# Kernel tuning notes

Measured on AMD Instinct MI355X. Metric: run time of the kernel, lower is better.

## Reference

```python
import jax, jax.numpy as jnp
import numpy as np

DIM = 1024
EXPAND = 2
HEAD_DIM = 64
D_STATE = 128
N_GROUPS = 1
D_CONV = 4
D_INNER = DIM * EXPAND            # 2048
N_HEADS = D_INNER // HEAD_DIM     # 32
CONV_DIM = D_INNER + 2 * N_GROUPS * D_STATE  # 2304
D_IN_PROJ = 2 * D_INNER + 2 * N_GROUPS * D_STATE + N_HEADS  # 4384
SEQLEN = 4096
LN_EPS = 1e-5


def setup_inputs() -> dict:
    key = jax.random.key(0)
    ks = jax.random.split(key, 6)
    x = jax.random.normal(ks[0], (SEQLEN, DIM), dtype=jnp.float32)
    W_in = jax.random.normal(ks[1], (D_IN_PROJ, DIM), dtype=jnp.float32) * 0.02
    conv_w = jax.random.normal(ks[2], (CONV_DIM, 1, D_CONV), dtype=jnp.float32) * 0.2
    conv_b = jax.random.normal(ks[3], (CONV_DIM,), dtype=jnp.float32) * 0.02
    # dt_bias init per module: dt ~ exp(U*(log(dt_max)-log(dt_min))+log(dt_min)); inv-softplus
    u = jax.random.uniform(ks[4], (N_HEADS,))
    dt = jnp.exp(u * (np.log(0.1) - np.log(0.001)) + np.log(0.001))
    dt = jnp.clip(dt, 1e-4)
    dt_bias = dt + jnp.log(-jnp.expm1(-dt))
    A_log = jnp.log(jax.random.uniform(ks[5], (N_HEADS,), minval=1.0, maxval=16.0))
    D = jnp.ones((N_HEADS,), dtype=jnp.float32)
    ln_w = jnp.ones((D_INNER,), dtype=jnp.float32)
    ln_b = jnp.zeros((D_INNER,), dtype=jnp.float32)
    W_out = jax.random.normal(jax.random.fold_in(key, 7), (DIM, D_INNER), dtype=jnp.float32) * 0.02
    return {"x": x, "W_in": W_in, "conv_w": conv_w, "conv_b": conv_b,
            "dt_bias": dt_bias, "A_log": A_log, "D": D,
            "ln_w": ln_w, "ln_b": ln_b, "W_out": W_out}


def _forward(x, W_in, conv_w, conv_b, dt_bias, A_log, D, ln_w, ln_b, W_out):
    L = x.shape[0]
    dtype = x.dtype
    A = -jnp.exp(A_log.astype(jnp.float32))  # (h,)
    zxbcdt = x @ W_in.T                       # (L, d_in_proj)
    z = zxbcdt[:, :D_INNER]                   # (L, d_inner)
    xbc = zxbcdt[:, D_INNER:D_INNER + CONV_DIM]
    dt = zxbcdt[:, -N_HEADS:]
    dt = jax.nn.softplus(dt.astype(jnp.float32) + dt_bias.astype(jnp.float32))  # (L, h)
    # depthwise 1D conv, SAME padding (module uses padding='SAME', then slices to L)
    xbc_c = jax.lax.conv_general_dilated(
        xbc.T[None],                          # (1, conv_dim, L)
        conv_w,                               # (conv_dim, 1, k)
        window_strides=(1,), padding='SAME',
        dimension_numbers=('NCH', 'OIH', 'NCH'),
        feature_group_count=CONV_DIM,
    )[0].T + conv_b                           # (L, conv_dim)
    xbc_s = jax.nn.silu(xbc_c)
    x_in = xbc_s[:, :D_INNER].reshape(L, N_HEADS, HEAD_DIM)      # (L, h, p)
    B = xbc_s[:, D_INNER:D_INNER + N_GROUPS * D_STATE]          # (L, n) with g=1
    C = xbc_s[:, D_INNER + N_GROUPS * D_STATE:]                 # (L, n)
    # non-causal linear attention (VSSD): y = C (B^T (x * dt * A)) + x * D
    dA = dt.astype(dtype) * A.astype(dtype)                     # (L, h)
    Vs = x_in * dA[..., None]                                   # (L, h, p)
    KV = jnp.einsum('ln,lhp->hnp', B, Vs)                       # (h, n, p)
    y = jnp.einsum('ln,hnp->lhp', C, KV) + x_in * D[None, :, None]
    y = y.reshape(L, D_INNER)
    # per-token LayerNorm, then multiplicative SiLU(z) gate
    mu = jnp.mean(y, axis=-1, keepdims=True)
    var = jnp.var(y, axis=-1, keepdims=True)
    yn = (y - mu) * jax.lax.rsqrt(var + LN_EPS) * ln_w + ln_b
    y = yn * jax.nn.silu(z)
    return y @ W_out.T                                          # (L, dim)


def reference(x, W_in, conv_w, conv_b, dt_bias, A_log, D, ln_w, ln_b, W_out):
    return _forward(x, W_in, conv_w, conv_b, dt_bias, A_log, D, ln_w, ln_b, W_out)
```

## Files before the change

### kernel.cpp

```cpp
#include <hip/hip_runtime.h>
#include <math.h>

#define SEQLEN    4096
#define DIM_IN    1024
#define D_INNER   2048
#define N_HEADS   32
#define D_STATE   128
#define CONV_DIM  2304
#define D_IN_PROJ 4384
#define PROJ_LD   4480
#define LN_EPS    1e-5f
#define KV_SPLIT  16

typedef __attribute__((ext_vector_type(8))) short bf16x8;
typedef __attribute__((ext_vector_type(4))) float f32x4;
typedef __attribute__((ext_vector_type(8))) short short8;

__device__ __forceinline__ ushort f2bf(float f) {
    union { float f; unsigned u; } v; v.f = f;
    unsigned u = v.u + 0x7FFFu + ((v.u >> 16) & 1u);
    return (ushort)(u >> 16);
}
__device__ __forceinline__ float bf2f(ushort h) {
    union { unsigned u; float f; } v; v.u = ((unsigned)h) << 16;
    return v.f;
}

__device__ __forceinline__ void gload16(const void* g, void* l) {
    __builtin_amdgcn_global_load_lds(
        (const __attribute__((address_space(1))) void*)g,
        (__attribute__((address_space(3))) void*)l, 16, 0, 0);
}

__global__ __launch_bounds__(256)
void cvt_bf16(const float* __restrict__ in, ushort* __restrict__ out, int n8) {
    int i = blockIdx.x * 256 + threadIdx.x;
    if (i >= n8) return;
    float4 v0 = reinterpret_cast<const float4*>(in)[i * 2];
    float4 v1 = reinterpret_cast<const float4*>(in)[i * 2 + 1];
    short8 r;
    r[0] = f2bf(v0.x); r[1] = f2bf(v0.y); r[2] = f2bf(v0.z); r[3] = f2bf(v0.w);
    r[4] = f2bf(v1.x); r[5] = f2bf(v1.y); r[6] = f2bf(v1.z); r[7] = f2bf(v1.w);
    *reinterpret_cast<short8*>(&out[i * 8]) = r;
}

__global__ __launch_bounds__(256)
void cvt_win(const float* __restrict__ in, ushort* __restrict__ out) {
    int i = blockIdx.x * 256 + threadIdx.x;
    const int n8 = PROJ_LD * DIM_IN / 8;
    if (i >= n8) return;
    int row = (i * 8) >> 10;
    short8 r;
    if (row < D_IN_PROJ) {
        float4 v0 = reinterpret_cast<const float4*>(in)[i * 2];
        float4 v1 = reinterpret_cast<const float4*>(in)[i * 2 + 1];
        r[0] = f2bf(v0.x); r[1] = f2bf(v0.y); r[2] = f2bf(v0.z); r[3] = f2bf(v0.w);
        r[4] = f2bf(v1.x); r[5] = f2bf(v1.y); r[6] = f2bf(v1.z); r[7] = f2bf(v1.w);
    } else {
        r = (short8){0,0,0,0,0,0,0,0};
    }
    *reinterpret_cast<short8*>(&out[i * 8]) = r;
}

template<int BN, int NT, int OUTBF>
__global__ __launch_bounds__(256)
void gemm_bf16_pipe(const ushort* __restrict__ A, int lda,
                    const ushort* __restrict__ B, int ldb,
                    void* __restrict__ Cout, int ldc) {
    constexpr int NI  = BN / 32;
    __shared__ ushort As[3][128 * 32];
    __shared__ ushort Bs[3][BN * 32];

    const int nwg = gridDim.x;
    const int wg  = blockIdx.x;
    const int swz = (wg & 7) * (nwg >> 3) + (wg >> 3);
    const int m0 = (swz & 31) * 128;
    const int n0 = (swz >> 5) * BN;

    const int tid  = threadIdx.x;
    const int wave = tid >> 6;
    const int lane = tid & 63;
    const int wm = (wave & 1) * 64;
    const int wn = (wave >> 1) * (BN / 2);
    const int r16 = lane & 15;
    const int kg  = lane >> 4;
    const int pkg = kg ^ ((r16 >> 1) & 3);

    f32x4 acc[4][NI];
    #pragma unroll
    for (int i = 0; i < 4; ++i)
        #pragma unroll
        for (int j = 0; j < NI; ++j) acc[i][j] = (f32x4){0.f, 0.f, 0.f, 0.f};

    const int srow = lane >> 2;
    const int scol = ((lane & 3) ^ ((lane >> 3) & 3)) * 8;
    const int ca0 = wave * 2, ca1 = wave * 2 + 1;
    const ushort* gA0 = A + (size_t)(m0 + ca0 * 16 + srow) * lda + scol;
    const ushort* gA1 = A + (size_t)(m0 + ca1 * 16 + srow) * lda + scol;
    const ushort* gB0;
    const ushort* gB1 = nullptr;
    int cb0, cb1 = 0;
    if constexpr (BN == 128) {
        cb0 = wave * 2; cb1 = wave * 2 + 1;
        gB0 = B + (size_t)(n0 + cb0 * 16 + srow) * ldb + scol;
        gB1 = B + (size_t)(n0 + cb1 * 16 + srow) * ldb + scol;
    } else {
        cb0 = wave;
        gB0 = B + (size_t)(n0 + cb0 * 16 + srow) * ldb + scol;
    }

#define STAGE_STEP(T, BUF)                                          \
    {                                                               \
        const int _k = (T) * 32;                                    \
        gload16(gA0 + _k, &As[BUF][ca0 * 512]);                     \
        gload16(gA1 + _k, &As[BUF][ca1 * 512]);                     \
        gload16(gB0 + _k, &Bs[BUF][cb0 * 512]);                     \
        if constexpr (BN == 128) gload16(gB1 + _k, &Bs[BUF][cb1 * 512]); \
    }

    STAGE_STEP(0, 0)
    STAGE_STEP(1, 1)

    int rb = 0;
    for (int t = 0; t < NT; ++t) {
        __builtin_amdgcn_sched_barrier(0);
        if (t + 1 < NT) {
            if constexpr (BN == 128) asm volatile("s_waitcnt vmcnt(4)" ::: "memory");
            else                     asm volatile("s_waitcnt vmcnt(3)" ::: "memory");
        } else {
            asm volatile("s_waitcnt vmcnt(0)" ::: "memory");
        }
        __builtin_amdgcn_s_barrier();
        __builtin_amdgcn_sched_barrier(0);

        if (t + 2 < NT) {
            int sb = rb + 2; if (sb >= 3) sb -= 3;
            STAGE_STEP(t + 2, sb)
        }

        const ushort* ab = &As[rb][0];
        const ushort* bb = &Bs[rb][0];
        bf16x8 a[4], b[NI];
        #pragma unroll
        for (int mi = 0; mi < 4; ++mi)
            a[mi] = *reinterpret_cast<const bf16x8*>(&ab[(wm + mi * 16 + r16) * 32 + pkg * 8]);
        #pragma unroll
        for (int ni = 0; ni < NI; ++ni)
            b[ni] = *reinterpret_cast<const bf16x8*>(&bb[(wn + ni * 16 + r16) * 32 + pkg * 8]);

        __builtin_amdgcn_s_setprio(1);
        #pragma unroll
        for (int mi = 0; mi < 4; ++mi)
            #pragma unroll
            for (int ni = 0; ni < NI; ++ni)
                acc[mi][ni] = __builtin_amdgcn_mfma_f32_16x16x32_bf16(a[mi], b[ni], acc[mi][ni], 0, 0, 0);
        __builtin_amdgcn_s_setprio(0);

        rb = (rb == 2) ? 0 : rb + 1;
    }
#undef STAGE_STEP

    if constexpr (OUTBF) {
        ushort* EP = &As[0][0];
        ushort* outp = (ushort*)Cout;
        __syncthreads();
        #pragma unroll
        for (int half = 0; half < 2; ++half) {
            if ((wave & 1) == half) {
                #pragma unroll
                for (int mi = 0; mi < 4; ++mi)
                    #pragma unroll
                    for (int ni = 0; ni < NI; ++ni)
                        #pragma unroll
                        for (int r = 0; r < 4; ++r)
                            EP[(mi * 16 + kg * 4 + r) * BN + wn + ni * 16 + r16] =
                                f2bf(acc[mi][ni][r]);
            }
            __syncthreads();
            #pragma unroll
            for (int i = 0; i < BN / 32; ++i) {
                int idx = tid + 256 * i;
                int row = idx / (BN / 8);
                int cb  = idx % (BN / 8);
                bf16x8 v = *reinterpret_cast<const bf16x8*>(&EP[row * BN + cb * 8]);
                *reinterpret_cast<bf16x8*>(
                    &outp[(size_t)(m0 + half * 64 + row) * ldc + n0 + cb * 8]) = v;
            }
            __syncthreads();
        }
    } else {
        float* outp = (float*)Cout;
        #pragma unroll
        for (int mi = 0; mi < 4; ++mi)
            #pragma unroll
            for (int ni = 0; ni < NI; ++ni)
                #pragma unroll
                for (int r = 0; r < 4; ++r) {
                    int row = m0 + wm + mi * 16 + kg * 4 + r;
                    int col = n0 + wn + ni * 16 + r16;
                    outp[(size_t)row * ldc + col] = acc[mi][ni][r];
                }
    }
}

__global__ __launch_bounds__(256)
void conv_silu_kernel(const ushort* __restrict__ zxb,
                      const float* __restrict__ conv_w,
                      const float* __restrict__ conv_b,
                      const float* __restrict__ dt_bias,
                      const float* __restrict__ A_log,
                      ushort* __restrict__ xbcs,
                      float* __restrict__ dA) {
    const int l = blockIdx.x;
    const ushort* base = zxb + (size_t)l * PROJ_LD + D_INNER;
    for (int c = threadIdx.x; c < CONV_DIM; c += 256) {
        float w0 = conv_w[c * 4 + 0], w1 = conv_w[c * 4 + 1];
        float w2 = conv_w[c * 4 + 2], w3 = conv_w[c * 4 + 3];
        float acc = conv_b[c];
        if (l >= 1)          acc += w0 * bf2f(base[c - PROJ_LD]);
        acc += w1 * bf2f(base[c]);
        if (l + 1 < SEQLEN)  acc += w2 * bf2f(base[c + PROJ_LD]);
        if (l + 2 < SEQLEN)  acc += w3 * bf2f(base[c + 2 * PROJ_LD]);
        float s = acc / (1.0f + expf(-acc));
        xbcs[(size_t)l * CONV_DIM + c] = f2bf(s);
    }
    if (threadIdx.x < N_HEADS) {
        int h = threadIdx.x;
        float v = bf2f(zxb[(size_t)l * PROJ_LD + (D_IN_PROJ - N_HEADS) + h]) + dt_bias[h];
        float sp = (v > 20.0f) ? v : log1pf(expf(v));
        dA[l * N_HEADS + h] = sp * (-expf(A_log[h]));
    }
}

__global__ __launch_bounds__(256)
void kv_kernel(const ushort* __restrict__ xbcs,
               const float* __restrict__ dA,
               float* __restrict__ KVp) {
    __shared__ float Vs[16][132];
    __shared__ float Bsm[16][132];
    const int hp0 = blockIdx.x * 128;
    const int lc0 = blockIdx.y * (SEQLEN / KV_SPLIT);
    const int tid = threadIdx.x;
    const int ty = tid >> 4, tx = tid & 15;
    float acc[8][8];
    #pragma unroll
    for (int i = 0; i < 8; ++i)
        #pragma unroll
        for (int j = 0; j < 8; ++j) acc[i][j] = 0.0f;

    for (int ls = 0; ls < SEQLEN / KV_SPLIT; ls += 16) {
        {
            int lrow = tid >> 4;
            int p8   = (tid & 15) * 8;
            int l = lc0 + ls + lrow;
            short8 v = *reinterpret_cast<const short8*>(
                &xbcs[(size_t)l * CONV_DIM + hp0 + p8]);
            float a = dA[l * N_HEADS + ((hp0 + p8) >> 6)];
            #pragma unroll
            for (int j = 0; j < 8; ++j) Vs[lrow][p8 + j] = bf2f((ushort)v[j]) * a;
            short8 b = *reinterpret_cast<const short8*>(
                &xbcs[(size_t)l * CONV_DIM + D_INNER + p8]);
            #pragma unroll
            for (int j = 0; j < 8; ++j) Bsm[lrow][p8 + j] = bf2f((ushort)b[j]);
        }
        __syncthreads();
        #pragma unroll
        for (int k = 0; k < 16; ++k) {
            float a[8], b[8];
            *reinterpret_cast<float4*>(&a[0]) = *reinterpret_cast<const float4*>(&Vs[k][ty * 8]);
            *reinterpret_cast<float4*>(&a[4]) = *reinterpret_cast<const float4*>(&Vs[k][ty * 8 + 4]);
            *reinterpret_cast<float4*>(&b[0]) = *reinterpret_cast<const float4*>(&Bsm[k][tx * 8]);
            *reinterpret_cast<float4*>(&b[4]) = *reinterpret_cast<const float4*>(&Bsm[k][tx * 8 + 4]);
            #pragma unroll
            for (int i = 0; i < 8; ++i)
                #pragma unroll
                for (int j = 0; j < 8; ++j)
                    acc[i][j] = fmaf(a[i], b[j], acc[i][j]);
        }
        __syncthreads();
    }
    float* dst = KVp + (size_t)blockIdx.y * (D_INNER * D_STATE);
    #pragma unroll
    for (int i = 0; i < 8; ++i) {
        int hp = hp0 + ty * 8 + i;
        #pragma unroll
        for (int j = 0; j < 8; j += 4) {
            float4 v = make_float4(acc[i][j], acc[i][j+1], acc[i][j+2], acc[i][j+3]);
            *reinterpret_cast<float4*>(&dst[(size_t)hp * D_STATE + tx * 8 + j]) = v;
        }
    }
}

__global__ __launch_bounds__(256)
void kv_reduce(const float* __restrict__ KVp, ushort* __restrict__ KVTb) {
    int i = blockIdx.x * 256 + threadIdx.x;
    float4 s = make_float4(0.f, 0.f, 0.f, 0.f);
    #pragma unroll
    for (int c = 0; c < KV_SPLIT; ++c) {
        float4 v = reinterpret_cast<const float4*>(KVp + (size_t)c * (D_INNER * D_STATE))[i];
        s.x += v.x; s.y += v.y; s.z += v.z; s.w += v.w;
    }
    ushort4 o;
    o.x = f2bf(s.x); o.y = f2bf(s.y); o.z = f2bf(s.z); o.w = f2bf(s.w);
    *reinterpret_cast<ushort4*>(&KVTb[i * 4]) = o;
}

__global__ __launch_bounds__(256)
void ln_gate_kernel(const ushort* __restrict__ y1b,
                    const ushort* __restrict__ xbcs,
                    const ushort* __restrict__ zxb,
                    const float* __restrict__ Dp,
                    const float* __restrict__ ln_w,
                    const float* __restrict__ ln_b,
                    ushort* __restrict__ yb) {
    const int l = blockIdx.x;
    const int tid = threadIdx.x;
    const int c = tid * 8;
    float y[8], z[8];
    float sum = 0.f, sumsq = 0.f;
    {
        short8 v  = *reinterpret_cast<const short8*>(&y1b[(size_t)l * D_INNER + c]);
        short8 xi = *reinterpret_cast<const short8*>(&xbcs[(size_t)l * CONV_DIM + c]);
        short8 zz = *reinterpret_cast<const short8*>(&zxb[(size_t)l * PROJ_LD + c]);
        float d = Dp[c >> 6];
        #pragma unroll
        for (int j = 0; j < 8; ++j) {
            float yv = bf2f((ushort)v[j]) + bf2f((ushort)xi[j]) * d;
            y[j] = yv;
            z[j] = bf2f((ushort)zz[j]);
            sum += yv;
            sumsq += yv * yv;
        }
    }
    #pragma unroll
    for (int off = 32; off > 0; off >>= 1) {
        sum   += __shfl_down(sum, off);
        sumsq += __shfl_down(sumsq, off);
    }
    __shared__ float red[8];
    int wid = tid >> 6;
    if ((tid & 63) == 0) { red[wid] = sum; red[4 + wid] = sumsq; }
    __syncthreads();
    sum   = red[0] + red[1] + red[2] + red[3];
    sumsq = red[4] + red[5] + red[6] + red[7];
    float mu  = sum * (1.0f / D_INNER);
    float var = sumsq * (1.0f / D_INNER) - mu * mu;
    float rs  = rsqrtf(var + LN_EPS);
    short8 o;
    #pragma unroll
    for (int j = 0; j < 8; ++j) {
        float yn = (y[j] - mu) * rs * ln_w[c + j] + ln_b[c + j];
        float g  = z[j] / (1.0f + expf(-z[j]));
        o[j] = f2bf(yn * g);
    }
    *reinterpret_cast<short8*>(&yb[(size_t)l * D_INNER + c]) = o;
}

extern "C" void kernel_launch(void* const* d_in, const int* in_sizes, int n_in,
                              void* d_out, int out_size, void* d_ws, size_t ws_size,
                              hipStream_t stream) {
    const float* x       = (const float*)d_in[0];
    const float* W_in    = (const float*)d_in[1];
    const float* conv_w  = (const float*)d_in[2];
    const float* conv_b  = (const float*)d_in[3];
    const float* dt_bias = (const float*)d_in[4];
    const float* A_log   = (const float*)d_in[5];
    const float* Dp      = (const float*)d_in[6];
    const float* ln_w    = (const float*)d_in[7];
    const float* ln_b    = (const float*)d_in[8];
    const float* W_out   = (const float*)d_in[9];
    float* out = (float*)d_out;

    char* ws = (char*)d_ws;
    ushort* zxb   = (ushort*)ws;
    ushort* xbcs  = (ushort*)(ws +  36700160);
    ushort* y1b   = (ushort*)(ws +  55574528);
    ushort* yb    = (ushort*)(ws +  72351744);
    float*  KVp   = (float*)(ws +  89128960);
    float*  dA    = (float*)(ws + 105906176);
    ushort* KVTb  = (ushort*)(ws + 106430464);
    ushort* Woutb = (ushort*)(ws + 106954752);
    ushort* xb    = (ushort*)(ws + 111149056);
    ushort* Winb  = (ushort*)(ws + 119537664);

    cvt_bf16<<<(SEQLEN * DIM_IN / 8 + 255) / 256, 256, 0, stream>>>(x, xb, SEQLEN * DIM_IN / 8);
    cvt_win<<<(PROJ_LD * DIM_IN / 8 + 255) / 256, 256, 0, stream>>>(W_in, Winb);
    cvt_bf16<<<(DIM_IN * D_INNER / 8 + 255) / 256, 256, 0, stream>>>(W_out, Woutb, DIM_IN * D_INNER / 8);

    gemm_bf16_pipe<128, 32, 1><<<(PROJ_LD / 128) * 32, 256, 0, stream>>>(
        xb, DIM_IN, Winb, DIM_IN, zxb, PROJ_LD);

    conv_silu_kernel<<<SEQLEN, 256, 0, stream>>>(zxb, conv_w, conv_b, dt_bias, A_log,
                                                 xbcs, dA);

    kv_kernel<<<dim3(16, KV_SPLIT), 256, 0, stream>>>(xbcs, dA, KVp);
    kv_reduce<<<(D_INNER * D_STATE / 4) / 256, 256, 0, stream>>>(KVp, KVTb);

    gemm_bf16_pipe<128, 4, 1><<<(D_INNER / 128) * 32, 256, 0, stream>>>(
        xbcs + (D_INNER + D_STATE), CONV_DIM, KVTb, D_STATE, y1b, D_INNER);

    ln_gate_kernel<<<SEQLEN, 256, 0, stream>>>(y1b, xbcs, zxb, Dp, ln_w, ln_b, yb);

    gemm_bf16_pipe<64, 64, 0><<<(DIM_IN / 64) * 32, 256, 0, stream>>>(
        yb, D_INNER, Woutb, D_INNER, out, DIM_IN);
}
```

Baseline: 224.7 us.

## Use 256x128 tile GEMM for input projection and pad epilogue LDS stride

```diff
diff --git a/kernel.cpp b/kernel.cpp
--- a/kernel.cpp
+++ b/kernel.cpp
@@ -62,14 +62,135 @@
     *reinterpret_cast<short8*>(&out[i * 8]) = r;
 }
 
+template<int NT>
+__global__ __launch_bounds__(256, 2)
+void gemm_bf16_big(const ushort* __restrict__ A, int lda,
+                   const ushort* __restrict__ B, int ldb,
+                   ushort* __restrict__ Cout, int ldc) {
+    __shared__ __align__(16) ushort S[3][12288];
+
+    const int nwg = gridDim.x;
+    const int wg  = blockIdx.x;
+    const int swz = (wg & 7) * (nwg >> 3) + (wg >> 3);
+    const int m0 = (swz & 15) * 256;
+    const int n0 = (swz >> 4) * 128;
+
+    const int tid  = threadIdx.x;
+    const int wave = tid >> 6;
+    const int lane = tid & 63;
+    const int wm = (wave >> 1) * 128;
+    const int wn = (wave & 1) * 64;
+    const int r16 = lane & 15;
+    const int kg  = lane >> 4;
+    const int pkg = kg ^ ((r16 >> 1) & 3);
+
+    f32x4 acc[8][4];
+    #pragma unroll
+    for (int i = 0; i < 8; ++i)
+        #pragma unroll
+        for (int j = 0; j < 4; ++j) acc[i][j] = (f32x4){0.f, 0.f, 0.f, 0.f};
+
+    const int srow = lane >> 2;
+    const int scol = ((lane & 3) ^ ((lane >> 3) & 3)) * 8;
+    const ushort* gsrc[6];
+    #pragma unroll
+    for (int i = 0; i < 6; ++i) {
+        int c = wave * 6 + i;
+        gsrc[i] = (c < 16)
+            ? A + (size_t)(m0 + c * 16 + srow) * lda + scol
+            : B + (size_t)(n0 + (c - 16) * 16 + srow) * ldb + scol;
+    }
+
+#define STAGE_BIG(T, BUF)                                            \
+    {                                                                \
+        const int _k = (T) * 32;                                     \
+        _Pragma("unroll")                                            \
+        for (int i = 0; i < 6; ++i)                                  \
+            gload16(gsrc[i] + _k, &S[BUF][(wave * 6 + i) * 512]);    \
+    }
+
+    STAGE_BIG(0, 0)
+    STAGE_BIG(1, 1)
+
+    int rb = 0;
+    for (int t = 0; t < NT; ++t) {
+        __builtin_amdgcn_sched_barrier(0);
+        if (t + 1 < NT) {
+            asm volatile("s_waitcnt vmcnt(6)" ::: "memory");
+        } else {
+            asm volatile("s_waitcnt vmcnt(0)" ::: "memory");
+        }
+        __builtin_amdgcn_s_barrier();
+        __builtin_amdgcn_sched_barrier(0);
+
+        if (t + 2 < NT) {
+            int sb = rb + 2; if (sb >= 3) sb -= 3;
+            STAGE_BIG(t + 2, sb)
+        }
+
+        const ushort* sp = &S[rb][0];
+        bf16x8 b4[4];
+        #pragma unroll
+        for (int ni = 0; ni < 4; ++ni)
+            b4[ni] = *reinterpret_cast<const bf16x8*>(
+                &sp[8192 + (wn + ni * 16 + r16) * 32 + pkg * 8]);
+        #pragma unroll
+        for (int mh = 0; mh < 2; ++mh) {
+            bf16x8 a4[4];
+            #pragma unroll
+            for (int i = 0; i < 4; ++i)
+                a4[i] = *reinterpret_cast<const bf16x8*>(
+                    &sp[(wm + (mh * 4 + i) * 16 + r16) * 32 + pkg * 8]);
+            __builtin_amdgcn_s_setprio(1);
+            #pragma unroll
+            for (int i = 0; i < 4; ++i)
+                #pragma unroll
+                for (int ni = 0; ni < 4; ++ni)
+                    acc[mh * 4 + i][ni] = __builtin_amdgcn_mfma_f32_16x16x32_bf16(
+                        a4[i], b4[ni], acc[mh * 4 + i][ni], 0, 0, 0);
+            __builtin_amdgcn_s_setprio(0);
+        }
+        rb = (rb == 2) ? 0 : rb + 1;
+    }
+#undef STAGE_BIG
+
+    ushort* EP = &S[0][0];
+    __syncthreads();
+    #pragma unroll
+    for (int half = 0; half < 2; ++half) {
+        if ((wave >> 1) == half) {
+            #pragma unroll
+            for (int mi = 0; mi < 8; ++mi)
+                #pragma unroll
+                for (int ni = 0; ni < 4; ++ni)
+                    #pragma unroll
+                    for (int r = 0; r < 4; ++r)
+                        EP[(mi * 16 + kg * 4 + r) * 136 + wn + ni * 16 + r16] =
+                            f2bf(acc[mi][ni][r]);
+        }
+        __syncthreads();
+        #pragma unroll
+        for (int i = 0; i < 8; ++i) {
+            int idx = tid + 256 * i;
+            int row = idx >> 4;
+            int cb  = idx & 15;
+            bf16x8 v = *reinterpret_cast<const bf16x8*>(&EP[row * 136 + cb * 8]);
+            *reinterpret_cast<bf16x8*>(
+                &Cout[(size_t)(m0 + half * 128 + row) * ldc + n0 + cb * 8]) = v;
+        }
+        __syncthreads();
+    }
+}
+
 template<int BN, int NT, int OUTBF>
 __global__ __launch_bounds__(256)
 void gemm_bf16_pipe(const ushort* __restrict__ A, int lda,
                     const ushort* __restrict__ B, int ldb,
                     void* __restrict__ Cout, int ldc) {
     constexpr int NI  = BN / 32;
-    __shared__ ushort As[3][128 * 32];
-    __shared__ ushort Bs[3][BN * 32];
+    constexpr int BNP = BN + 8;
+    __shared__ __align__(16) ushort As[3][128 * 32];
+    __shared__ __align__(16) ushort Bs[3][BN * 32];
 
     const int nwg = gridDim.x;
     const int wg  = blockIdx.x;
@@ -173,7 +294,7 @@
                     for (int ni = 0; ni < NI; ++ni)
                         #pragma unroll
                         for (int r = 0; r < 4; ++r)
-                            EP[(mi * 16 + kg * 4 + r) * BN + wn + ni * 16 + r16] =
+                            EP[(mi * 16 + kg * 4 + r) * BNP + wn + ni * 16 + r16] =
                                 f2bf(acc[mi][ni][r]);
             }
             __syncthreads();
@@ -182,7 +303,7 @@
                 int idx = tid + 256 * i;
                 int row = idx / (BN / 8);
                 int cb  = idx % (BN / 8);
-                bf16x8 v = *reinterpret_cast<const bf16x8*>(&EP[row * BN + cb * 8]);
+                bf16x8 v = *reinterpret_cast<const bf16x8*>(&EP[row * BNP + cb * 8]);
                 *reinterpret_cast<bf16x8*>(
                     &outp[(size_t)(m0 + half * 64 + row) * ldc + n0 + cb * 8]) = v;
             }
@@ -387,7 +508,7 @@
     cvt_win<<<(PROJ_LD * DIM_IN / 8 + 255) / 256, 256, 0, stream>>>(W_in, Winb);
     cvt_bf16<<<(DIM_IN * D_INNER / 8 + 255) / 256, 256, 0, stream>>>(W_out, Woutb, DIM_IN * D_INNER / 8);
 
-    gemm_bf16_pipe<128, 32, 1><<<(PROJ_LD / 128) * 32, 256, 0, stream>>>(
+    gemm_bf16_big<32><<<16 * (PROJ_LD / 128), 256, 0, stream>>>(
         xb, DIM_IN, Winb, DIM_IN, zxb, PROJ_LD);
 
     conv_silu_kernel<<<SEQLEN, 256, 0, stream>>>(zxb, conv_w, conv_b, dt_bias, A_log,
```

New measurement: 208.2 us. 1.08x faster.
